# Optimization experiments

Hardware: AMD Instinct MI355X
Metric: run time of the kernel (lower is better)

## Reference

```python
import jax, jax.numpy as jnp
import numpy as np

N = 40000          # nodes
E = 640000         # edges (avg degree 16)
D_MODEL = 128
H = 8              # num_heads
DH = 16            # d_head
DFF = 512
CLAMP = 5.0
EPS = 1e-5


def setup_inputs() -> dict:
    key = jax.random.key(0)
    ks = jax.random.split(key, 10)
    s = 0.08  # weight init scale
    return {
        "feat": jax.random.normal(ks[0], (N, D_MODEL), dtype=jnp.float32),
        "src": jax.random.randint(ks[1], (E,), 0, N, dtype=jnp.int32),
        "dst": jax.random.randint(ks[2], (E,), 0, N, dtype=jnp.int32),
        "Wq": jax.random.normal(ks[3], (H * DH, D_MODEL), dtype=jnp.float32) * s,
        "Wk": jax.random.normal(ks[4], (H * DH, D_MODEL), dtype=jnp.float32) * s,
        "Wv": jax.random.normal(ks[5], (H * DH, D_MODEL), dtype=jnp.float32) * s,
        "Wo": jax.random.normal(ks[6], (D_MODEL, H * DH), dtype=jnp.float32) * s,
        "ln1_g": jnp.ones((D_MODEL,), jnp.float32),
        "ln1_b": jnp.zeros((D_MODEL,), jnp.float32),
        "W1": jax.random.normal(ks[7], (DFF, D_MODEL), dtype=jnp.float32) * s,
        "b1": jnp.zeros((DFF,), jnp.float32),
        "W2": jax.random.normal(ks[8], (D_MODEL, DFF), dtype=jnp.float32) * s,
        "b2": jnp.zeros((D_MODEL,), jnp.float32),
        "ln2_g": jnp.ones((D_MODEL,), jnp.float32),
        "ln2_b": jnp.zeros((D_MODEL,), jnp.float32),
    }


def _layer_norm(x, g, b):
    mu = jnp.mean(x, axis=-1, keepdims=True)
    var = jnp.mean(jnp.square(x - mu), axis=-1, keepdims=True)
    return (x - mu) * jax.lax.rsqrt(var + EPS) * g + b


def reference(feat, src, dst, Wq, Wk, Wv, Wo, ln1_g, ln1_b, W1, b1, W2, b2, ln2_g, ln2_b):
    n = feat.shape[0]
    # Node-level projections (equivalent to DGL's per-edge Linear on gathered feats)
    q = (feat @ Wq.T).reshape(n, H, DH)
    k = (feat @ Wk.T).reshape(n, H, DH)
    v = (feat @ Wv.T).reshape(n, H, DH)

    # Per-edge multi-head attention logits: q[dst] . k[src] / sqrt(d_head), clamped
    u = jnp.sum(q[dst] * k[src], axis=-1) / np.sqrt(DH)   # [E, H]
    u = jnp.clip(u, -CLAMP, CLAMP)

    # Ragged edge-softmax over incoming edges of each dst node
    m = jax.ops.segment_max(u, dst, num_segments=n)        # [N, H]
    e = jnp.exp(u - m[dst])                                # [E, H]
    denom = jax.ops.segment_sum(e, dst, num_segments=n)    # [N, H]
    a = e / denom[dst]                                     # [E, H]

    # Weighted V scatter-reduce back to dst nodes
    av = (a[:, :, None] * v[src]).reshape(-1, H * DH)      # [E, H*DH]
    sum_av = jax.ops.segment_sum(av, dst, num_segments=n)  # [N, H*DH]
    uh = sum_av @ Wo.T                                     # [N, d_model]

    h1 = _layer_norm(feat + uh, ln1_g, ln1_b)
    ffn = jax.nn.relu(h1 @ W1.T + b1) @ W2.T + b2
    return _layer_norm(h1 + ffn, ln2_g, ln2_b)
```

## Files before the change

### kernel.cpp

```cpp
#include <hip/hip_runtime.h>

#define DM 128
#define DFF 512
#define CLAMP_V 5.0f
#define LN_EPS 1e-5f

typedef __attribute__((ext_vector_type(8))) short bf16x8;
typedef __attribute__((ext_vector_type(4))) float f32x4;

__device__ __forceinline__ float b2f(ushort u) {
  union { uint u; float f; } x; x.u = ((uint)u) << 16; return x.f;
}
__device__ __forceinline__ ushort f2b(float f) {
  union { float f; uint u; } x; x.f = f;
  uint r = x.u + 0x7FFFu + ((x.u >> 16) & 1u);
  return (ushort)(r >> 16);
}
__device__ __forceinline__ void unpackw(uint w, float& lo, float& hi) {
  union { uint u; float f; } A, B;
  A.u = w << 16; B.u = w & 0xFFFF0000u;
  lo = A.f; hi = B.f;
}
__device__ __forceinline__ void unpack8w(uint4 w, float* o) {
  unpackw(w.x, o[0], o[1]); unpackw(w.y, o[2], o[3]);
  unpackw(w.z, o[4], o[5]); unpackw(w.w, o[6], o[7]);
}

__global__ void k_cast(const float* __restrict__ s, ushort* __restrict__ d, int n) {
  int i4 = (blockIdx.x * blockDim.x + threadIdx.x) * 4;
  if (i4 + 3 < n) {
    float4 v = *reinterpret_cast<const float4*>(s + i4);
    ushort4 o; o.x = f2b(v.x); o.y = f2b(v.y); o.z = f2b(v.z); o.w = f2b(v.w);
    *reinterpret_cast<ushort4*>(d + i4) = o;
  } else {
    for (; i4 < n; ++i4) d[i4] = f2b(s[i4]);
  }
}

__global__ void k_castw(const float* __restrict__ wq, const float* __restrict__ wk,
                        const float* __restrict__ wv, const float* __restrict__ wo,
                        const float* __restrict__ w1, const float* __restrict__ w2,
                        ushort* __restrict__ d) {
  int i4 = (blockIdx.x * blockDim.x + threadIdx.x) * 4;
  if (i4 >= 196608) return;
  const float* s; int o;
  if      (i4 < 16384)  { s = wq; o = i4; }
  else if (i4 < 32768)  { s = wk; o = i4 - 16384; }
  else if (i4 < 49152)  { s = wv; o = i4 - 32768; }
  else if (i4 < 65536)  { s = wo; o = i4 - 49152; }
  else if (i4 < 131072) { s = w1; o = i4 - 65536; }
  else                  { s = w2; o = i4 - 131072; }
  float4 v = *reinterpret_cast<const float4*>(s + o);
  ushort4 u; u.x = f2b(v.x); u.y = f2b(v.y); u.z = f2b(v.z); u.w = f2b(v.w);
  *reinterpret_cast<ushort4*>(d + i4) = u;
}

__global__ void k_count(const int* __restrict__ dst, int* __restrict__ deg, int E) {
  int e = blockIdx.x * blockDim.x + threadIdx.x;
  if (e < E) atomicAdd(&deg[dst[e]], 1);
}

#define SC_EPB 1024

__global__ __launch_bounds__(256) void k_scan1(const int* __restrict__ deg,
                                               int* __restrict__ off,
                                               int* __restrict__ bsum, int n) {
  __shared__ int sh[256];
  const int t = threadIdx.x;
  int base = blockIdx.x * SC_EPB + t * 4;
  int4 v = {0, 0, 0, 0};
  if (base + 3 < n) {
    v = *reinterpret_cast<const int4*>(deg + base);
  } else {
    if (base     < n) v.x = deg[base];
    if (base + 1 < n) v.y = deg[base + 1];
    if (base + 2 < n) v.z = deg[base + 2];
    if (base + 3 < n) v.w = deg[base + 3];
  }
  int s = v.x + v.y + v.z + v.w;
  sh[t] = s;
  __syncthreads();
  #pragma unroll
  for (int d = 1; d < 256; d <<= 1) {
    int x = 0;
    if (t >= d) x = sh[t - d];
    __syncthreads();
    sh[t] += x;
    __syncthreads();
  }
  int ex = sh[t] - s;
  if (base + 3 < n) {
    int4 o; o.x = ex; o.y = ex + v.x; o.z = ex + v.x + v.y; o.w = ex + v.x + v.y + v.z;
    *reinterpret_cast<int4*>(off + base) = o;
  } else {
    if (base     < n) off[base]     = ex;
    if (base + 1 < n) off[base + 1] = ex + v.x;
    if (base + 2 < n) off[base + 2] = ex + v.x + v.y;
    if (base + 3 < n) off[base + 3] = ex + v.x + v.y + v.z;
  }
  if (t == 255) bsum[blockIdx.x] = sh[255];
}

__global__ __launch_bounds__(256) void k_scan2(int* __restrict__ bsum, int nb) {
  __shared__ int sh[256];
  const int t = threadIdx.x;
  int v = (t < nb) ? bsum[t] : 0;
  sh[t] = v;
  __syncthreads();
  #pragma unroll
  for (int d = 1; d < 256; d <<= 1) {
    int x = 0;
    if (t >= d) x = sh[t - d];
    __syncthreads();
    sh[t] += x;
    __syncthreads();
  }
  if (t < nb) bsum[t] = sh[t] - v;
}

__global__ __launch_bounds__(256) void k_scan3(int* __restrict__ off,
                                               const int* __restrict__ bsum,
                                               int n, int E) {
  int add = bsum[blockIdx.x];
  int base = blockIdx.x * SC_EPB + threadIdx.x * 4;
  if (base + 3 < n) {
    int4 v = *reinterpret_cast<int4*>(off + base);
    v.x += add; v.y += add; v.z += add; v.w += add;
    *reinterpret_cast<int4*>(off + base) = v;
  } else {
    if (base     < n) off[base]     += add;
    if (base + 1 < n) off[base + 1] += add;
    if (base + 2 < n) off[base + 2] += add;
  }
  if (blockIdx.x == 0 && threadIdx.x == 0) off[n] = E;
}

__global__ void k_scatter(const int* __restrict__ src, const int* __restrict__ dst,
                          const int* __restrict__ off, int* __restrict__ cur,
                          int* __restrict__ csr, int E) {
  int e = blockIdx.x * blockDim.x + threadIdx.x;
  if (e < E) {
    int d = dst[e];
    int p = off[d] + atomicAdd(&cur[d], 1);
    csr[p] = src[e];
  }
}

template<int FLAGS, bool QKVSPLIT, bool OUTF, bool OUTB>
__global__ __launch_bounds__(512, 1) void k_mmS(
    const ushort* __restrict__ A, const ushort* __restrict__ W,
    const float* __restrict__ bias, const float* __restrict__ res,
    const float* __restrict__ lng, const float* __restrict__ lnbv,
    float* __restrict__ Cf, ushort* __restrict__ Cb, ushort* __restrict__ Cb2,
    int M, int ldc)
{
  __shared__ ushort Bs[128 * 128];
  __shared__ ushort As[2][128 * 128];
  __shared__ float lnred[(FLAGS & 8) ? 1024 : 4];

  const int tid = threadIdx.x;
  const int wv = tid >> 6, ln = tid & 63;
  const int bnb = blockIdx.x;
  const int wrow = (wv >> 2) * 64, wcol = (wv & 3) * 32;
  const int o_base = wv * 1024 + ln * 16;

  const int nT = (M + 127) >> 7;
  const int T = (nT + gridDim.y - 1) / gridDim.y;
  const int t0 = blockIdx.y * T;
  const int t1 = min(t0 + T, nT);
  if (t0 >= nT) return;

  #pragma unroll
  for (int is = 0; is < 4; ++is) {
    int o = is * 8192 + o_base;
    int row = o >> 8;
    int c = ((o >> 4) & 15) ^ (row & 15);
    const ushort* s = W + (size_t)(bnb * 128 + row) * 128 + c * 8;
    __builtin_amdgcn_global_load_lds(
        (const __attribute__((address_space(1))) void*)s,
        (__attribute__((address_space(3))) void*)((char*)Bs + is * 8192 + wv * 1024),
        16, 0, 0);
  }
  {
    #pragma unroll
    for (int is = 0; is < 4; ++is) {
      int o = is * 8192 + o_base;
      int row = o >> 8;
      int c = ((o >> 4) & 15) ^ (row & 15);
      int gr = min(t0 * 128 + row, M - 1);
      const ushort* s = A + (size_t)gr * 128 + c * 8;
      __builtin_amdgcn_global_load_lds(
          (const __attribute__((address_space(1))) void*)s,
          (__attribute__((address_space(3))) void*)((char*)As[0] + is * 8192 + wv * 1024),
          16, 0, 0);
    }
  }
  __syncthreads();

  int buf = 0;
  for (int t = t0; t < t1; ++t) {
    if (t + 1 < t1) {
      #pragma unroll
      for (int is = 0; is < 4; ++is) {
        int o = is * 8192 + o_base;
        int row = o >> 8;
        int c = ((o >> 4) & 15) ^ (row & 15);
        int gr = min((t + 1) * 128 + row, M - 1);
        const ushort* s = A + (size_t)gr * 128 + c * 8;
        __builtin_amdgcn_global_load_lds(
            (const __attribute__((address_space(1))) void*)s,
            (__attribute__((address_space(3))) void*)((char*)As[buf ^ 1] + is * 8192 + wv * 1024),
            16, 0, 0);
      }
    }

    f32x4 acc[4][2] = {};
    const char* AsB = (const char*)As[buf];
    const char* BsB = (const char*)Bs;
    #pragma unroll
    for (int kk = 0; kk < 4; ++kk) {
      bf16x8 af[4], bfr[2];
      #pragma unroll
      for (int m = 0; m < 4; ++m) {
        int r = wrow + m * 16 + (ln & 15);
        int c = kk * 4 + (ln >> 4);
        af[m] = *reinterpret_cast<const bf16x8*>(AsB + r * 256 + ((c ^ (r & 15)) << 4));
      }
      #pragma unroll
      for (int n = 0; n < 2; ++n) {
        int r = wcol + n * 16 + (ln & 15);
        int c = kk * 4 + (ln >> 4);
        bfr[n] = *reinterpret_cast<const bf16x8*>(BsB + r * 256 + ((c ^ (r & 15)) << 4));
      }
      #pragma unroll
      for (int m = 0; m < 4; ++m)
        #pragma unroll
        for (int n = 0; n < 2; ++n)
          acc[m][n] = __builtin_amdgcn_mfma_f32_16x16x32_bf16(af[m], bfr[n], acc[m][n], 0, 0, 0);
    }

    const int mbase = t * 128;
    if constexpr ((FLAGS & 8) != 0) {
      #pragma unroll
      for (int m = 0; m < 4; ++m)
        #pragma unroll
        for (int n = 0; n < 2; ++n) {
          int gc = wcol + n * 16 + (ln & 15);
          #pragma unroll
          for (int r = 0; r < 4; ++r) {
            int gr = mbase + wrow + m * 16 + (ln >> 4) * 4 + r;
            float v = acc[m][n][r];
            if (FLAGS & 1) v += bias[gc];
            if (FLAGS & 2) v = fmaxf(v, 0.f);
            if (FLAGS & 4) v += res[(size_t)min(gr, M - 1) * 128 + gc];
            acc[m][n][r] = v;
          }
        }
      #pragma unroll
      for (int m = 0; m < 4; ++m)
        #pragma unroll
        for (int r = 0; r < 4; ++r) {
          float sm = acc[m][0][r] + acc[m][1][r];
          float sq = acc[m][0][r] * acc[m][0][r] + acc[m][1][r] * acc[m][1][r];
          #pragma unroll
          for (int msk = 1; msk <= 8; msk <<= 1) {
            sm += __shfl_xor(sm, msk);
            sq += __shfl_xor(sq, msk);
          }
          if ((ln & 15) == 0) {
            int row = wrow + m * 16 + (ln >> 4) * 4 + r;
            lnred[row * 8 + (wv & 3) * 2]     = sm;
            lnred[row * 8 + (wv & 3) * 2 + 1] = sq;
          }
        }
      __syncthreads();
      #pragma unroll
      for (int m = 0; m < 4; ++m)
        #pragma unroll
        for (int r = 0; r < 4; ++r) {
          int row = wrow + m * 16 + (ln >> 4) * 4 + r;
          int gr = mbase + row;
          float sm = lnred[row * 8] + lnred[row * 8 + 2] + lnred[row * 8 + 4] + lnred[row * 8 + 6];
          float sq = lnred[row * 8 + 1] + lnred[row * 8 + 3] + lnred[row * 8 + 5] + lnred[row * 8 + 7];
          float mu = sm * (1.f / 128.f);
          float var = fmaxf(sq * (1.f / 128.f) - mu * mu, 0.f);
          float rstd = rsqrtf(var + LN_EPS);
          if (gr < M) {
            #pragma unroll
            for (int n = 0; n < 2; ++n) {
              int gc = wcol + n * 16 + (ln & 15);
              float y = (acc[m][n][r] - mu) * rstd * lng[gc] + lnbv[gc];
              if (OUTF) Cf[(size_t)gr * 128 + gc] = y;
              if (OUTB) Cb[(size_t)gr * 128 + gc] = f2b(y);
            }
          }
        }
    } else {
      #pragma unroll
      for (int m = 0; m < 4; ++m) {
        int gr0 = mbase + wrow + m * 16 + (ln >> 4) * 4;
        #pragma unroll
        for (int n = 0; n < 2; ++n) {
          int gcl = wcol + n * 16 + (ln & 15);
          float bsv = (FLAGS & 1) ? bias[bnb * 128 + gcl] : 0.f;
          #pragma unroll
          for (int r = 0; r < 4; ++r) {
            int gr = gr0 + r;
            if (gr >= M) continue;
            float v = acc[m][n][r] + bsv;
            if (FLAGS & 2) v = fmaxf(v, 0.f);
            if (QKVSPLIT) {
              if (bnb == 0) Cb[(size_t)gr * 128 + gcl] = f2b(v);
              else          Cb2[(size_t)gr * 256 + (bnb - 1) * 128 + gcl] = f2b(v);
            } else {
              if (OUTF) Cf[(size_t)gr * ldc + bnb * 128 + gcl] = v;
              if (OUTB) Cb[(size_t)gr * ldc + bnb * 128 + gcl] = f2b(v);
            }
          }
        }
      }
    }
    __syncthreads();
    buf ^= 1;
  }
}

#define BM 128
#define BN 128
#define BK 64

template<int FLAGS, bool OUTF, bool OUTB>
__global__ __launch_bounds__(256, 2) void k_mm2(
    const ushort* __restrict__ A, const ushort* __restrict__ W,
    const float* __restrict__ bias, const float* __restrict__ res,
    const float* __restrict__ lng, const float* __restrict__ lnbv,
    float* __restrict__ Cf, ushort* __restrict__ Cb,
    int M, int NO, int K)
{
  __shared__ ushort As[2][BM * BK];
  __shared__ ushort Ws[2][BN * BK];
  __shared__ float lnred[(FLAGS & 8) ? 512 : 4];

  const int tid = threadIdx.x;
  const int wv = tid >> 6, ln = tid & 63;
  const int bm = blockIdx.y * BM, bn = blockIdx.x * BN;
  const int wrow = (wv >> 1) * 64, wcol = (wv & 1) * 64;
  const int o_base = wv * 1024 + ln * 16;

  auto STG = [&](int kidx, int b) {
    #pragma unroll
    for (int is = 0; is < 4; ++is) {
      int o = is * 4096 + o_base;
      int row = o >> 7;
      int c = ((o >> 4) & 7) ^ (row & 7);
      int gm = min(bm + row, M - 1);
      const ushort* sA = A + (size_t)gm * K + kidx * BK + c * 8;
      __builtin_amdgcn_global_load_lds(
          (const __attribute__((address_space(1))) void*)sA,
          (__attribute__((address_space(3))) void*)((char*)As[b] + is * 4096 + wv * 1024),
          16, 0, 0);
      int gn = bn + row;
      const ushort* sW = W + (size_t)gn * K + kidx * BK + c * 8;
      __builtin_amdgcn_global_load_lds(
          (const __attribute__((address_space(1))) void*)sW,
          (__attribute__((address_space(3))) void*)((char*)Ws[b] + is * 4096 + wv * 1024),
          16, 0, 0);
    }
  };

  f32x4 acc[4][4] = {};
  const int KT = K >> 6;
  STG(0, 0);
  __syncthreads();
  int buf = 0;
  for (int i = 0; i < KT; ++i) {
    if (i + 1 < KT) STG(i + 1, buf ^ 1);
    const char* AsB = (const char*)As[buf];
    const char* WsB = (const char*)Ws[buf];
    #pragma unroll
    for (int kk = 0; kk < 2; ++kk) {
      bf16x8 af[4], bfr[4];
      #pragma unroll
      for (int m = 0; m < 4; ++m) {
        int r = wrow + m * 16 + (ln & 15);
        int c = kk * 4 + (ln >> 4);
        af[m] = *reinterpret_cast<const bf16x8*>(AsB + r * 128 + ((c ^ (r & 7)) << 4));
      }
      #pragma unroll
      for (int n = 0; n < 4; ++n) {
        int r = wcol + n * 16 + (ln & 15);
        int c = kk * 4 + (ln >> 4);
        bfr[n] = *reinterpret_cast<const bf16x8*>(WsB + r * 128 + ((c ^ (r & 7)) << 4));
      }
      #pragma unroll
      for (int m = 0; m < 4; ++m)
        #pragma unroll
        for (int n = 0; n < 4; ++n)
          acc[m][n] = __builtin_amdgcn_mfma_f32_16x16x32_bf16(af[m], bfr[n], acc[m][n], 0, 0, 0);
    }
    __syncthreads();
    buf ^= 1;
  }

  if constexpr ((FLAGS & 8) != 0) {
    #pragma unroll
    for (int m = 0; m < 4; ++m)
      #pragma unroll
      for (int n = 0; n < 4; ++n) {
        int gc = wcol + n * 16 + (ln & 15);
        float bsv = (FLAGS & 1) ? bias[gc] : 0.f;
        #pragma unroll
        for (int r = 0; r < 4; ++r) {
          int gr = bm + wrow + m * 16 + (ln >> 4) * 4 + r;
          float v = acc[m][n][r] + bsv;
          if (FLAGS & 2) v = fmaxf(v, 0.f);
          if (FLAGS & 4) v += res[(size_t)min(gr, M - 1) * 128 + gc];
          acc[m][n][r] = v;
        }
      }
    #pragma unroll
    for (int m = 0; m < 4; ++m)
      #pragma unroll
      for (int r = 0; r < 4; ++r) {
        float sm = acc[m][0][r] + acc[m][1][r] + acc[m][2][r] + acc[m][3][r];
        float sq = acc[m][0][r] * acc[m][0][r] + acc[m][1][r] * acc[m][1][r]
                 + acc[m][2][r] * acc[m][2][r] + acc[m][3][r] * acc[m][3][r];
        #pragma unroll
        for (int msk = 1; msk <= 8; msk <<= 1) {
          sm += __shfl_xor(sm, msk);
          sq += __shfl_xor(sq, msk);
        }
        if ((ln & 15) == 0) {
          int row = wrow + m * 16 + (ln >> 4) * 4 + r;
          lnred[row * 4 + (wv & 1) * 2]     = sm;
          lnred[row * 4 + (wv & 1) * 2 + 1] = sq;
        }
      }
    __syncthreads();
    #pragma unroll
    for (int m = 0; m < 4; ++m)
      #pragma unroll
      for (int r = 0; r < 4; ++r) {
        int row = wrow + m * 16 + (ln >> 4) * 4 + r;
        int gr = bm + row;
        float sm = lnred[row * 4] + lnred[row * 4 + 2];
        float sq = lnred[row * 4 + 1] + lnred[row * 4 + 3];
        float mu = sm * (1.f / 128.f);
        float var = fmaxf(sq * (1.f / 128.f) - mu * mu, 0.f);
        float rstd = rsqrtf(var + LN_EPS);
        if (gr < M) {
          #pragma unroll
          for (int n = 0; n < 4; ++n) {
            int gc = wcol + n * 16 + (ln & 15);
            float y = (acc[m][n][r] - mu) * rstd * lng[gc] + lnbv[gc];
            if (OUTF) Cf[(size_t)gr * 128 + gc] = y;
            if (OUTB) Cb[(size_t)gr * 128 + gc] = f2b(y);
          }
        }
      }
  } else {
    #pragma unroll
    for (int m = 0; m < 4; ++m) {
      int gr0 = bm + wrow + m * 16 + (ln >> 4) * 4;
      #pragma unroll
      for (int n = 0; n < 4; ++n) {
        int gc = bn + wcol + n * 16 + (ln & 15);
        float bsv = (FLAGS & 1) ? bias[gc] : 0.f;
        #pragma unroll
        for (int r = 0; r < 4; ++r) {
          int gr = gr0 + r;
          if (gr >= M) continue;
          float v = acc[m][n][r] + bsv;
          if (FLAGS & 2) v = fmaxf(v, 0.f);
          if (FLAGS & 4) v += res[(size_t)gr * NO + gc];
          if (OUTF) Cf[(size_t)gr * NO + gc] = v;
          if (OUTB) Cb[(size_t)gr * NO + gc] = f2b(v);
        }
      }
    }
  }
}

__global__ __launch_bounds__(256) void k_attn(
    const ushort* __restrict__ q, const ushort* __restrict__ kv,
    const int* __restrict__ off, const int* __restrict__ csr,
    ushort* __restrict__ sav, int n)
{
  int node = blockIdx.x * 4 + (threadIdx.x >> 6);
  int lane = threadIdx.x & 63;
  if (node >= n) return;
  const int g = lane >> 3, sl = lane & 7;

  const ushort* qr = q + (size_t)node * 128 + sl * 16;
  uint4 qw0 = *reinterpret_cast<const uint4*>(qr);
  uint4 qw1 = *reinterpret_cast<const uint4*>(qr + 8);
  float qv[16];
  unpack8w(qw0, qv); unpack8w(qw1, qv + 8);

  int b = off[node], e = off[node + 1];
  float s = 0.f;
  float a[16] = {};
  int nIt = (e - b + 7) >> 3;
  int idx = b + g;
  int sn = (b < e) ? csr[min(idx, e - 1)] : 0;

  for (int i = 0; i < nIt; ++i) {
    bool act = idx < e;
    const ushort* kr = kv + (size_t)sn * 256 + sl * 16;
    uint4 kw0 = *reinterpret_cast<const uint4*>(kr);
    uint4 kw1 = *reinterpret_cast<const uint4*>(kr + 8);
    uint4 vw0 = *reinterpret_cast<const uint4*>(kr + 128);
    uint4 vw1 = *reinterpret_cast<const uint4*>(kr + 136);
    idx += 8;
    if (i + 1 < nIt) sn = csr[min(idx, e - 1)];

    float kk[16];
    unpack8w(kw0, kk); unpack8w(kw1, kk + 8);
    float p = 0.f;
    #pragma unroll
    for (int j = 0; j < 16; ++j) p = fmaf(qv[j], kk[j], p);
    float u = fminf(fmaxf(p * 0.25f, -CLAMP_V), CLAMP_V);
    float w = __expf(u - CLAMP_V);
    w = act ? w : 0.f;
    s += w;
    float vvv[16];
    unpack8w(vw0, vvv); unpack8w(vw1, vvv + 8);
    #pragma unroll
    for (int j = 0; j < 16; ++j) a[j] = fmaf(w, vvv[j], a[j]);
  }

  #pragma unroll
  for (int msk = 8; msk <= 32; msk <<= 1) {
    s += __shfl_xor(s, msk);
    #pragma unroll
    for (int j = 0; j < 16; ++j) a[j] += __shfl_xor(a[j], msk);
  }

  float inv = (s > 0.f) ? 1.f / s : 0.f;
  if (g == 0) {
    uint w[8];
    #pragma unroll
    for (int j = 0; j < 8; ++j)
      w[j] = (uint)f2b(a[2 * j] * inv) | ((uint)f2b(a[2 * j + 1] * inv) << 16);
    ushort* outp = sav + (size_t)node * 128 + sl * 16;
    uint4 o0 = {w[0], w[1], w[2], w[3]};
    uint4 o1 = {w[4], w[5], w[6], w[7]};
    *reinterpret_cast<uint4*>(outp) = o0;
    *reinterpret_cast<uint4*>(outp + 8) = o1;
  }
}

extern "C" void kernel_launch(void* const* d_in, const int* in_sizes, int n_in,
                              void* d_out, int out_size, void* d_ws, size_t ws_size,
                              hipStream_t stream)
{
  const float* feat = (const float*)d_in[0];
  const int*   src  = (const int*)d_in[1];
  const int*   dst  = (const int*)d_in[2];
  const float* Wq   = (const float*)d_in[3];
  const float* Wk   = (const float*)d_in[4];
  const float* Wv   = (const float*)d_in[5];
  const float* Wo   = (const float*)d_in[6];
  const float* ln1g = (const float*)d_in[7];
  const float* ln1b = (const float*)d_in[8];
  const float* W1   = (const float*)d_in[9];
  const float* b1   = (const float*)d_in[10];
  const float* W2   = (const float*)d_in[11];
  const float* b2   = (const float*)d_in[12];
  const float* ln2g = (const float*)d_in[13];
  const float* ln2b = (const float*)d_in[14];
  float* out = (float*)d_out;

  const int N = in_sizes[0] / DM;
  const int E = in_sizes[1];
  const size_t NB = (size_t)N;

  char* wsb = (char*)d_ws;
  ushort* q_bf    = (ushort*)wsb;
  ushort* kv_bf   = (ushort*)(wsb + NB * 256);
  ushort* sav_bf  = (ushort*)(wsb + NB * 768);
  ushort* mid_bf  = (ushort*)wsb;
  float*  h1      = (float*)(wsb + NB * 1024);
  ushort* h1b     = (ushort*)(wsb + NB * 1536);
  ushort* feat_bf = (ushort*)(wsb + NB * 1792);
  ushort* wbf     = (ushort*)(wsb + NB * 2048);
  ushort* wqkv_bf = wbf;
  ushort* wo_bf   = wbf + 49152;
  ushort* w1_bf   = wbf + 65536;
  ushort* w2_bf   = wbf + 131072;
  int* ib  = (int*)(wbf + 196608);
  int* deg = ib;
  int* cur = ib + N;
  int* off = ib + 2 * N;
  int* csr = ib + 3 * N + 1;
  int* bsum = csr + E;

  hipMemsetAsync(deg, 0, 2 * (size_t)N * sizeof(int), stream);

  int nf = N * DM;
  k_cast<<<(nf / 4 + 255) / 256, 256, 0, stream>>>(feat, feat_bf, nf);
  k_castw<<<192, 256, 0, stream>>>(Wq, Wk, Wv, Wo, W1, W2, wbf);

  int eb = (E + 255) / 256;
  int nbk = (N + SC_EPB - 1) / SC_EPB;
  k_count<<<eb, 256, 0, stream>>>(dst, deg, E);
  k_scan1<<<nbk, 256, 0, stream>>>(deg, off, bsum, N);
  k_scan2<<<1, 256, 0, stream>>>(bsum, nbk);
  k_scan3<<<nbk, 256, 0, stream>>>(off, bsum, N, E);
  k_scatter<<<eb, 256, 0, stream>>>(src, dst, off, cur, csr, E);

  int nb4 = (N + 3) / 4;
  const int nT = (N + 127) / 128;

  {
    int S = (nT + 3) / 4;
    k_mmS<0, true, false, true><<<dim3(3, S), 512, 0, stream>>>(
        feat_bf, wqkv_bf, nullptr, nullptr, nullptr, nullptr,
        nullptr, q_bf, kv_bf, N, 0);
  }

  k_attn<<<nb4, 256, 0, stream>>>(q_bf, kv_bf, off, csr, sav_bf, N);

  {
    int S = (nT + 1) / 2;
    k_mmS<4 | 8, false, true, true><<<dim3(1, S), 512, 0, stream>>>(
        sav_bf, wo_bf, nullptr, feat, ln1g, ln1b, h1, h1b, nullptr, N, 128);
  }

  {
    int S = (nT + 4) / 5;
    k_mmS<1 | 2, false, false, true><<<dim3(4, S), 512, 0, stream>>>(
        h1b, w1_bf, b1, nullptr, nullptr, nullptr,
        nullptr, mid_bf, nullptr, N, DFF);
  }

  k_mm2<1 | 4 | 8, true, false><<<dim3(1, nT), 256, 0, stream>>>(
      mid_bf, w2_bf, b2, h1, ln2g, ln2b, out, nullptr, N, DM, DFF);
}
```

Measured before the change: 199.9 us.

## Use one-tile-per-block GEMMs and software-pipeline attention gathers

```diff
diff --git a/kernel.cpp b/kernel.cpp
--- a/kernel.cpp
+++ b/kernel.cpp
@@ -147,181 +147,147 @@
 }
 
 template<int FLAGS, bool QKVSPLIT, bool OUTF, bool OUTB>
-__global__ __launch_bounds__(512, 1) void k_mmS(
+__global__ __launch_bounds__(512, 4) void k_mmT(
     const ushort* __restrict__ A, const ushort* __restrict__ W,
     const float* __restrict__ bias, const float* __restrict__ res,
     const float* __restrict__ lng, const float* __restrict__ lnbv,
     float* __restrict__ Cf, ushort* __restrict__ Cb, ushort* __restrict__ Cb2,
     int M, int ldc)
 {
+  __shared__ ushort As[128 * 128];
   __shared__ ushort Bs[128 * 128];
-  __shared__ ushort As[2][128 * 128];
   __shared__ float lnred[(FLAGS & 8) ? 1024 : 4];
 
   const int tid = threadIdx.x;
   const int wv = tid >> 6, ln = tid & 63;
   const int bnb = blockIdx.x;
+  const int mbase = blockIdx.y * 128;
   const int wrow = (wv >> 2) * 64, wcol = (wv & 3) * 32;
-  const int o_base = wv * 1024 + ln * 16;
-
-  const int nT = (M + 127) >> 7;
-  const int T = (nT + gridDim.y - 1) / gridDim.y;
-  const int t0 = blockIdx.y * T;
-  const int t1 = min(t0 + T, nT);
-  if (t0 >= nT) return;
+  const int o_base = tid * 16;
 
   #pragma unroll
   for (int is = 0; is < 4; ++is) {
     int o = is * 8192 + o_base;
     int row = o >> 8;
     int c = ((o >> 4) & 15) ^ (row & 15);
-    const ushort* s = W + (size_t)(bnb * 128 + row) * 128 + c * 8;
+    int gr = min(mbase + row, M - 1);
+    const ushort* sA = A + (size_t)gr * 128 + c * 8;
     __builtin_amdgcn_global_load_lds(
-        (const __attribute__((address_space(1))) void*)s,
+        (const __attribute__((address_space(1))) void*)sA,
+        (__attribute__((address_space(3))) void*)((char*)As + is * 8192 + wv * 1024),
+        16, 0, 0);
+    const ushort* sB = W + (size_t)(bnb * 128 + row) * 128 + c * 8;
+    __builtin_amdgcn_global_load_lds(
+        (const __attribute__((address_space(1))) void*)sB,
         (__attribute__((address_space(3))) void*)((char*)Bs + is * 8192 + wv * 1024),
         16, 0, 0);
   }
-  {
-    #pragma unroll
-    for (int is = 0; is < 4; ++is) {
-      int o = is * 8192 + o_base;
-      int row = o >> 8;
-      int c = ((o >> 4) & 15) ^ (row & 15);
-      int gr = min(t0 * 128 + row, M - 1);
-      const ushort* s = A + (size_t)gr * 128 + c * 8;
-      __builtin_amdgcn_global_load_lds(
-          (const __attribute__((address_space(1))) void*)s,
-          (__attribute__((address_space(3))) void*)((char*)As[0] + is * 8192 + wv * 1024),
-          16, 0, 0);
+  __syncthreads();
+
+  f32x4 acc[4][2] = {};
+  const char* AsB = (const char*)As;
+  const char* BsB = (const char*)Bs;
+  #pragma unroll
+  for (int kk = 0; kk < 4; ++kk) {
+    bf16x8 af[4], bfr[2];
+    #pragma unroll
+    for (int m = 0; m < 4; ++m) {
+      int r = wrow + m * 16 + (ln & 15);
+      int c = kk * 4 + (ln >> 4);
+      af[m] = *reinterpret_cast<const bf16x8*>(AsB + r * 256 + ((c ^ (r & 15)) << 4));
     }
-  }
-  __syncthreads();
-
-  int buf = 0;
-  for (int t = t0; t < t1; ++t) {
-    if (t + 1 < t1) {
-      #pragma unroll
-      for (int is = 0; is < 4; ++is) {
-        int o = is * 8192 + o_base;
-        int row = o >> 8;
-        int c = ((o >> 4) & 15) ^ (row & 15);
-        int gr = min((t + 1) * 128 + row, M - 1);
-        const ushort* s = A + (size_t)gr * 128 + c * 8;
-        __builtin_amdgcn_global_load_lds(
-            (const __attribute__((address_space(1))) void*)s,
-            (__attribute__((address_space(3))) void*)((char*)As[buf ^ 1] + is * 8192 + wv * 1024),
-            16, 0, 0);
-      }
+    #pragma unroll
+    for (int n = 0; n < 2; ++n) {
+      int r = wcol + n * 16 + (ln & 15);
+      int c = kk * 4 + (ln >> 4);
+      bfr[n] = *reinterpret_cast<const bf16x8*>(BsB + r * 256 + ((c ^ (r & 15)) << 4));
     }
-
-    f32x4 acc[4][2] = {};
-    const char* AsB = (const char*)As[buf];
-    const char* BsB = (const char*)Bs;
-    #pragma unroll
-    for (int kk = 0; kk < 4; ++kk) {
-      bf16x8 af[4], bfr[2];
-      #pragma unroll
-      for (int m = 0; m < 4; ++m) {
-        int r = wrow + m * 16 + (ln & 15);
-        int c = kk * 4 + (ln >> 4);
-        af[m] = *reinterpret_cast<const bf16x8*>(AsB + r * 256 + ((c ^ (r & 15)) << 4));
-      }
+    #pragma unroll
+    for (int m = 0; m < 4; ++m)
+      #pragma unroll
+      for (int n = 0; n < 2; ++n)
+        acc[m][n] = __builtin_amdgcn_mfma_f32_16x16x32_bf16(af[m], bfr[n], acc[m][n], 0, 0, 0);
+  }
+
+  if constexpr ((FLAGS & 8) != 0) {
+    #pragma unroll
+    for (int m = 0; m < 4; ++m)
       #pragma unroll
       for (int n = 0; n < 2; ++n) {
-        int r = wcol + n * 16 + (ln & 15);
-        int c = kk * 4 + (ln >> 4);
-        bfr[n] = *reinterpret_cast<const bf16x8*>(BsB + r * 256 + ((c ^ (r & 15)) << 4));
-      }
-      #pragma unroll
-      for (int m = 0; m < 4; ++m)
-        #pragma unroll
-        for (int n = 0; n < 2; ++n)
-          acc[m][n] = __builtin_amdgcn_mfma_f32_16x16x32_bf16(af[m], bfr[n], acc[m][n], 0, 0, 0);
-    }
-
-    const int mbase = t * 128;
-    if constexpr ((FLAGS & 8) != 0) {
-      #pragma unroll
-      for (int m = 0; m < 4; ++m)
-        #pragma unroll
-        for (int n = 0; n < 2; ++n) {
-          int gc = wcol + n * 16 + (ln & 15);
-          #pragma unroll
-          for (int r = 0; r < 4; ++r) {
-            int gr = mbase + wrow + m * 16 + (ln >> 4) * 4 + r;
-            float v = acc[m][n][r];
-            if (FLAGS & 1) v += bias[gc];
-            if (FLAGS & 2) v = fmaxf(v, 0.f);
-            if (FLAGS & 4) v += res[(size_t)min(gr, M - 1) * 128 + gc];
-            acc[m][n][r] = v;
-          }
-        }
-      #pragma unroll
-      for (int m = 0; m < 4; ++m)
+        int gc = wcol + n * 16 + (ln & 15);
         #pragma unroll
         for (int r = 0; r < 4; ++r) {
-          float sm = acc[m][0][r] + acc[m][1][r];
-          float sq = acc[m][0][r] * acc[m][0][r] + acc[m][1][r] * acc[m][1][r];
+          int gr = mbase + wrow + m * 16 + (ln >> 4) * 4 + r;
+          float v = acc[m][n][r];
+          if (FLAGS & 1) v += bias[gc];
+          if (FLAGS & 2) v = fmaxf(v, 0.f);
+          if (FLAGS & 4) v += res[(size_t)min(gr, M - 1) * 128 + gc];
+          acc[m][n][r] = v;
+        }
+      }
+    #pragma unroll
+    for (int m = 0; m < 4; ++m)
+      #pragma unroll
+      for (int r = 0; r < 4; ++r) {
+        float sm = acc[m][0][r] + acc[m][1][r];
+        float sq = acc[m][0][r] * acc[m][0][r] + acc[m][1][r] * acc[m][1][r];
+        #pragma unroll
+        for (int msk = 1; msk <= 8; msk <<= 1) {
+          sm += __shfl_xor(sm, msk);
+          sq += __shfl_xor(sq, msk);
+        }
+        if ((ln & 15) == 0) {
+          int row = wrow + m * 16 + (ln >> 4) * 4 + r;
+          lnred[row * 8 + (wv & 3) * 2]     = sm;
+          lnred[row * 8 + (wv & 3) * 2 + 1] = sq;
+        }
+      }
+    __syncthreads();
+    #pragma unroll
+    for (int m = 0; m < 4; ++m)
+      #pragma unroll
+      for (int r = 0; r < 4; ++r) {
+        int row = wrow + m * 16 + (ln >> 4) * 4 + r;
+        int gr = mbase + row;
+        float sm = lnred[row * 8] + lnred[row * 8 + 2] + lnred[row * 8 + 4] + lnred[row * 8 + 6];
+        float sq = lnred[row * 8 + 1] + lnred[row * 8 + 3] + lnred[row * 8 + 5] + lnred[row * 8 + 7];
+        float mu = sm * (1.f / 128.f);
+        float var = fmaxf(sq * (1.f / 128.f) - mu * mu, 0.f);
+        float rstd = rsqrtf(var + LN_EPS);
+        if (gr < M) {
           #pragma unroll
-          for (int msk = 1; msk <= 8; msk <<= 1) {
-            sm += __shfl_xor(sm, msk);
-            sq += __shfl_xor(sq, msk);
+          for (int n = 0; n < 2; ++n) {
+            int gc = wcol + n * 16 + (ln & 15);
+            float y = (acc[m][n][r] - mu) * rstd * lng[gc] + lnbv[gc];
+            if (OUTF) Cf[(size_t)gr * 128 + gc] = y;
+            if (OUTB) Cb[(size_t)gr * 128 + gc] = f2b(y);
           }
-          if ((ln & 15) == 0) {
-            int row = wrow + m * 16 + (ln >> 4) * 4 + r;
-            lnred[row * 8 + (wv & 3) * 2]     = sm;
-            lnred[row * 8 + (wv & 3) * 2 + 1] = sq;
-          }
-        }
-      __syncthreads();
-      #pragma unroll
-      for (int m = 0; m < 4; ++m)
+        }
+      }
+  } else {
+    #pragma unroll
+    for (int m = 0; m < 4; ++m) {
+      int gr0 = mbase + wrow + m * 16 + (ln >> 4) * 4;
+      #pragma unroll
+      for (int n = 0; n < 2; ++n) {
+        int gcl = wcol + n * 16 + (ln & 15);
+        float bsv = (FLAGS & 1) ? bias[bnb * 128 + gcl] : 0.f;
         #pragma unroll
         for (int r = 0; r < 4; ++r) {
-          int row = wrow + m * 16 + (ln >> 4) * 4 + r;
-          int gr = mbase + row;
-          float sm = lnred[row * 8] + lnred[row * 8 + 2] + lnred[row * 8 + 4] + lnred[row * 8 + 6];
-          float sq = lnred[row * 8 + 1] + lnred[row * 8 + 3] + lnred[row * 8 + 5] + lnred[row * 8 + 7];
-          float mu = sm * (1.f / 128.f);
-          float var = fmaxf(sq * (1.f / 128.f) - mu * mu, 0.f);
-          float rstd = rsqrtf(var + LN_EPS);
-          if (gr < M) {
-            #pragma unroll
-            for (int n = 0; n < 2; ++n) {
-              int gc = wcol + n * 16 + (ln & 15);
-              float y = (acc[m][n][r] - mu) * rstd * lng[gc] + lnbv[gc];
-              if (OUTF) Cf[(size_t)gr * 128 + gc] = y;
-              if (OUTB) Cb[(size_t)gr * 128 + gc] = f2b(y);
-            }
+          int gr = gr0 + r;
+          if (gr >= M) continue;
+          float v = acc[m][n][r] + bsv;
+          if (FLAGS & 2) v = fmaxf(v, 0.f);
+          if (QKVSPLIT) {
+            if (bnb == 0) Cb[(size_t)gr * 128 + gcl] = f2b(v);
+            else          Cb2[(size_t)gr * 256 + (bnb - 1) * 128 + gcl] = f2b(v);
+          } else {
+            if (OUTF) Cf[(size_t)gr * ldc + bnb * 128 + gcl] = v;
+            if (OUTB) Cb[(size_t)gr * ldc + bnb * 128 + gcl] = f2b(v);
           }
         }
-    } else {
-      #pragma unroll
-      for (int m = 0; m < 4; ++m) {
-        int gr0 = mbase + wrow + m * 16 + (ln >> 4) * 4;
-        #pragma unroll
-        for (int n = 0; n < 2; ++n) {
-          int gcl = wcol + n * 16 + (ln & 15);
-          float bsv = (FLAGS & 1) ? bias[bnb * 128 + gcl] : 0.f;
-          #pragma unroll
-          for (int r = 0; r < 4; ++r) {
-            int gr = gr0 + r;
-            if (gr >= M) continue;
-            float v = acc[m][n][r] + bsv;
-            if (FLAGS & 2) v = fmaxf(v, 0.f);
-            if (QKVSPLIT) {
-              if (bnb == 0) Cb[(size_t)gr * 128 + gcl] = f2b(v);
-              else          Cb2[(size_t)gr * 256 + (bnb - 1) * 128 + gcl] = f2b(v);
-            } else {
-              if (OUTF) Cf[(size_t)gr * ldc + bnb * 128 + gcl] = v;
-              if (OUTB) Cb[(size_t)gr * ldc + bnb * 128 + gcl] = f2b(v);
-            }
-          }
-        }
       }
     }
-    __syncthreads();
-    buf ^= 1;
   }
 }
 
@@ -501,32 +467,63 @@
   float s = 0.f;
   float a[16] = {};
   int nIt = (e - b + 7) >> 3;
-  int idx = b + g;
-  int sn = (b < e) ? csr[min(idx, e - 1)] : 0;
-
-  for (int i = 0; i < nIt; ++i) {
-    bool act = idx < e;
-    const ushort* kr = kv + (size_t)sn * 256 + sl * 16;
-    uint4 kw0 = *reinterpret_cast<const uint4*>(kr);
-    uint4 kw1 = *reinterpret_cast<const uint4*>(kr + 8);
-    uint4 vw0 = *reinterpret_cast<const uint4*>(kr + 128);
-    uint4 vw1 = *reinterpret_cast<const uint4*>(kr + 136);
-    idx += 8;
-    if (i + 1 < nIt) sn = csr[min(idx, e - 1)];
-
-    float kk[16];
-    unpack8w(kw0, kk); unpack8w(kw1, kk + 8);
-    float p = 0.f;
-    #pragma unroll
-    for (int j = 0; j < 16; ++j) p = fmaf(qv[j], kk[j], p);
-    float u = fminf(fmaxf(p * 0.25f, -CLAMP_V), CLAMP_V);
-    float w = __expf(u - CLAMP_V);
-    w = act ? w : 0.f;
-    s += w;
-    float vvv[16];
-    unpack8w(vw0, vvv); unpack8w(vw1, vvv + 8);
-    #pragma unroll
-    for (int j = 0; j < 16; ++j) a[j] = fmaf(w, vvv[j], a[j]);
+
+  if (nIt > 0) {
+    int idx = b + g;
+    int snA = csr[min(idx, e - 1)];
+    const ushort* krA = kv + (size_t)snA * 256 + sl * 16;
+    uint4 kA0 = *reinterpret_cast<const uint4*>(krA);
+    uint4 kA1 = *reinterpret_cast<const uint4*>(krA + 8);
+    uint4 vA0 = *reinterpret_cast<const uint4*>(krA + 128);
+    uint4 vA1 = *reinterpret_cast<const uint4*>(krA + 136);
+    int snB = (nIt > 1) ? csr[min(idx + 8, e - 1)] : 0;
+    uint4 kB0, kB1, vB0, vB1;
+    int i = 0;
+
+    #define ATT_COMPUTE(K0, K1, V0, V1)                                  \
+      {                                                                  \
+        float kk[16];                                                    \
+        unpack8w(K0, kk); unpack8w(K1, kk + 8);                          \
+        float p = 0.f;                                                   \
+        _Pragma("unroll")                                                \
+        for (int j = 0; j < 16; ++j) p = fmaf(qv[j], kk[j], p);          \
+        float u = fminf(fmaxf(p * 0.25f, -CLAMP_V), CLAMP_V);            \
+        float w = __expf(u - CLAMP_V);                                   \
+        w = (idx < e) ? w : 0.f;                                         \
+        s += w;                                                          \
+        float vvv[16];                                                   \
+        unpack8w(V0, vvv); unpack8w(V1, vvv + 8);                        \
+        _Pragma("unroll")                                                \
+        for (int j = 0; j < 16; ++j) a[j] = fmaf(w, vvv[j], a[j]);       \
+      }
+
+    while (true) {
+      if (i + 1 < nIt) {
+        const ushort* kr = kv + (size_t)snB * 256 + sl * 16;
+        kB0 = *reinterpret_cast<const uint4*>(kr);
+        kB1 = *reinterpret_cast<const uint4*>(kr + 8);
+        vB0 = *reinterpret_cast<const uint4*>(kr + 128);
+        vB1 = *reinterpret_cast<const uint4*>(kr + 136);
+      }
+      int snC = (i + 2 < nIt) ? csr[min(idx + 16, e - 1)] : 0;
+      ATT_COMPUTE(kA0, kA1, vA0, vA1)
+      idx += 8; ++i;
+      if (i >= nIt) break;
+
+      if (i + 1 < nIt) {
+        const ushort* kr = kv + (size_t)snC * 256 + sl * 16;
+        kA0 = *reinterpret_cast<const uint4*>(kr);
+        kA1 = *reinterpret_cast<const uint4*>(kr + 8);
+        vA0 = *reinterpret_cast<const uint4*>(kr + 128);
+        vA1 = *reinterpret_cast<const uint4*>(kr + 136);
+      }
+      int snD = (i + 2 < nIt) ? csr[min(idx + 16, e - 1)] : 0;
+      ATT_COMPUTE(kB0, kB1, vB0, vB1)
+      idx += 8; ++i;
+      if (i >= nIt) break;
+      snB = snD;
+    }
+    #undef ATT_COMPUTE
   }
 
   #pragma unroll
@@ -612,27 +609,18 @@
   int nb4 = (N + 3) / 4;
   const int nT = (N + 127) / 128;
 
-  {
-    int S = (nT + 3) / 4;
-    k_mmS<0, true, false, true><<<dim3(3, S), 512, 0, stream>>>(
-        feat_bf, wqkv_bf, nullptr, nullptr, nullptr, nullptr,
-        nullptr, q_bf, kv_bf, N, 0);
-  }
+  k_mmT<0, true, false, true><<<dim3(3, nT), 512, 0, stream>>>(
+      feat_bf, wqkv_bf, nullptr, nullptr, nullptr, nullptr,
+      nullptr, q_bf, kv_bf, N, 128);
 
   k_attn<<<nb4, 256, 0, stream>>>(q_bf, kv_bf, off, csr, sav_bf, N);
 
-  {
-    int S = (nT + 1) / 2;
-    k_mmS<4 | 8, false, true, true><<<dim3(1, S), 512, 0, stream>>>(
-        sav_bf, wo_bf, nullptr, feat, ln1g, ln1b, h1, h1b, nullptr, N, 128);
-  }
-
-  {
-    int S = (nT + 4) / 5;
-    k_mmS<1 | 2, false, false, true><<<dim3(4, S), 512, 0, stream>>>(
-        h1b, w1_bf, b1, nullptr, nullptr, nullptr,
-        nullptr, mid_bf, nullptr, N, DFF);
-  }
+  k_mmT<4 | 8, false, true, true><<<dim3(1, nT), 512, 0, stream>>>(
+      sav_bf, wo_bf, nullptr, feat, ln1g, ln1b, h1, h1b, nullptr, N, 128);
+
+  k_mmT<1 | 2, false, false, true><<<dim3(4, nT), 512, 0, stream>>>(
+      h1b, w1_bf, b1, nullptr, nullptr, nullptr,
+      nullptr, mid_bf, nullptr, N, DFF);
 
   k_mm2<1 | 4 | 8, true, false><<<dim3(1, nT), 256, 0, stream>>>(
       mid_bf, w2_bf, b2, h1, ln2g, ln2b, out, nullptr, N, DM, DFF);
```

Result: no change. 203.0 us (+1.5%).
